# Optimization experiments

Measured on AMD Instinct MI355X. Metric: run time of the kernel, lower is better.

The kernel has to match this reference:

```python
import jax, jax.numpy as jnp
import numpy as np

N_NODES = 50000
N_EDGES = 800000
D_IN = 64
D_OUT = 64


def setup_inputs() -> dict:
    key = jax.random.key(0)
    k1, k2, k3, k4, k5 = jax.random.split(key, 5)
    features = jax.random.normal(k1, (N_NODES, D_IN), dtype=jnp.float32)
    edge_src = jax.random.randint(k2, (N_EDGES,), 0, N_NODES, dtype=jnp.int32)
    edge_dst = jax.random.randint(k3, (N_EDGES,), 0, N_NODES, dtype=jnp.int32)
    edge_weight = jax.random.uniform(k4, (N_EDGES,), dtype=jnp.float32)
    # Linear(2*D_IN, D_OUT): weight [D_OUT, 2*D_IN], bias [D_OUT]
    W = jax.random.normal(k5, (D_OUT, 2 * D_IN), dtype=jnp.float32) * (1.0 / np.sqrt(2 * D_IN))
    b = jnp.zeros((D_OUT,), dtype=jnp.float32)
    return {"features": features, "edge_src": edge_src, "edge_dst": edge_dst,
            "edge_weight": edge_weight, "W": W, "b": b}


def reference(features, edge_src, edge_dst, edge_weight, W, b):
    n = features.shape[0]
    # spmm(adj, features): out[i] = sum_j adj[i,j] * features[j]
    gathered = features[edge_src] * edge_weight[:, None]          # [E, D_IN]
    neighbor = jax.ops.segment_sum(gathered, edge_dst, num_segments=n)  # [N, D_IN]
    combined = jnp.concatenate([features, neighbor], axis=1)     # [N, 2*D_IN]
    out = combined @ W.T + b                                      # [N, D_OUT]
    # F.normalize(p=2, dim=1): x / max(||x||, 1e-12)
    norm = jnp.maximum(jnp.linalg.norm(out, axis=1, keepdims=True), 1e-12)
    return out / norm
```

## Files before the change

### kernel.cpp

```cpp
#include <hip/hip_runtime.h>

#define D 64
#define TILE 1024
#define RB 8
#define EPB 2048
#define EPT 8

__global__ __launch_bounds__(256) void hist_kernel(
    const int* __restrict__ edge_dst, int* __restrict__ deg,
    int n_edges, int n_nodes)
{
    __shared__ int s_cnt;
    __shared__ int s_d[EPB];
    int r = blockIdx.x & (RB - 1);
    int chunk = blockIdx.x >> 3;
    int lo = (int)((long long)r * n_nodes / RB);
    int hi = (int)((long long)(r + 1) * n_nodes / RB);
    if (threadIdx.x == 0) s_cnt = 0;
    __syncthreads();

    int base = chunk * EPB + threadIdx.x * EPT;
    int d[EPT];
    if (base + EPT - 1 < n_edges) {
        int4 v0 = *(const int4*)(edge_dst + base);
        int4 v1 = *(const int4*)(edge_dst + base + 4);
        d[0]=v0.x; d[1]=v0.y; d[2]=v0.z; d[3]=v0.w;
        d[4]=v1.x; d[5]=v1.y; d[6]=v1.z; d[7]=v1.w;
    } else {
        #pragma unroll
        for (int k = 0; k < EPT; ++k)
            d[k] = (base + k < n_edges) ? edge_dst[base + k] : -1;
    }

    int lane = threadIdx.x & 63;
    unsigned long long lt = (lane == 63) ? ~0ull >> 1
                                         : ((1ull << (lane + 1)) - 1) >> 1;
    #pragma unroll
    for (int k = 0; k < EPT; ++k) {
        bool m = (d[k] >= lo && d[k] < hi);
        unsigned long long bal = __ballot(m);
        int cw = __popcll(bal);
        if (cw) {
            int bs = 0;
            if (lane == 0) bs = atomicAdd(&s_cnt, cw);
            bs = __builtin_amdgcn_readfirstlane(bs);
            if (m) s_d[bs + __popcll(bal & lt)] = d[k];
        }
    }
    __syncthreads();
    int c = s_cnt;
    for (int i = threadIdx.x; i < c; i += 256) atomicAdd(&deg[s_d[i]], 1);
}

__global__ __launch_bounds__(256) void tile_sum_kernel(
    const int* __restrict__ deg, int* __restrict__ partial, int n)
{
    int t = threadIdx.x;
    int base = blockIdx.x * TILE + t * 4;
    int s = 0;
    if (base + 3 < n) {
        int4 v = *(const int4*)(deg + base);
        s = v.x + v.y + v.z + v.w;
    } else {
        for (int k = 0; k < 4; ++k) if (base + k < n) s += deg[base + k];
    }
    #pragma unroll
    for (int off = 1; off < 64; off <<= 1) s += __shfl_xor(s, off, 64);
    __shared__ int wsum[4];
    int lane = t & 63, wv = t >> 6;
    if (lane == 0) wsum[wv] = s;
    __syncthreads();
    if (t == 0) partial[blockIdx.x] = wsum[0] + wsum[1] + wsum[2] + wsum[3];
}

__global__ __launch_bounds__(64) void scan_partial_kernel(
    const int* __restrict__ partial, int* __restrict__ ppref, int nb,
    int* __restrict__ offsets, int n, int n_edges)
{
    int lane = threadIdx.x;
    int carry = 0;
    for (int base = 0; base < nb; base += 64) {
        int idx = base + lane;
        int v = (idx < nb) ? partial[idx] : 0;
        int inc = v;
        #pragma unroll
        for (int off = 1; off < 64; off <<= 1) {
            int u = __shfl_up(inc, off, 64);
            if (lane >= off) inc += u;
        }
        if (idx < nb) ppref[idx] = carry + inc - v;
        carry += __shfl(inc, 63, 64);
    }
    if (lane == 0) offsets[n] = n_edges;
}

__global__ __launch_bounds__(256) void scan_tile_kernel(
    const int* __restrict__ deg, const int* __restrict__ ppref,
    int* __restrict__ offsets, int* __restrict__ cursor, int n)
{
    int t = threadIdx.x;
    int base = blockIdx.x * TILE + t * 4;
    int e0 = 0, e1 = 0, e2 = 0, e3 = 0;
    if (base + 3 < n) {
        int4 v = *(const int4*)(deg + base);
        e0 = v.x; e1 = v.y; e2 = v.z; e3 = v.w;
    } else {
        if (base + 0 < n) e0 = deg[base + 0];
        if (base + 1 < n) e1 = deg[base + 1];
        if (base + 2 < n) e2 = deg[base + 2];
        if (base + 3 < n) e3 = deg[base + 3];
    }
    int s = e0 + e1 + e2 + e3;
    int inc = s;
    int lane = t & 63, wv = t >> 6;
    #pragma unroll
    for (int off = 1; off < 64; off <<= 1) {
        int u = __shfl_up(inc, off, 64);
        if (lane >= off) inc += u;
    }
    __shared__ int wsum[4];
    if (lane == 63) wsum[wv] = inc;
    __syncthreads();
    int wpre = 0;
    for (int wq = 0; wq < wv; ++wq) wpre += wsum[wq];
    int excl = ppref[blockIdx.x] + wpre + inc - s;
    int o0 = excl, o1 = o0 + e0, o2 = o1 + e1, o3 = o2 + e2;
    if (base + 0 < n) { offsets[base + 0] = o0; cursor[base + 0] = o0; }
    if (base + 1 < n) { offsets[base + 1] = o1; cursor[base + 1] = o1; }
    if (base + 2 < n) { offsets[base + 2] = o2; cursor[base + 2] = o2; }
    if (base + 3 < n) { offsets[base + 3] = o3; cursor[base + 3] = o3; }
}

__global__ __launch_bounds__(256) void fill_kernel(
    const int* __restrict__ edge_src, const int* __restrict__ edge_dst,
    const float* __restrict__ edge_weight,
    int* __restrict__ cursor, int2* __restrict__ csr_sw,
    int n_edges, int n_nodes)
{
    __shared__ int s_cnt;
    __shared__ int s_d[EPB];
    __shared__ int s_e[EPB];
    int r = blockIdx.x & (RB - 1);
    int chunk = blockIdx.x >> 3;
    int lo = (int)((long long)r * n_nodes / RB);
    int hi = (int)((long long)(r + 1) * n_nodes / RB);
    if (threadIdx.x == 0) s_cnt = 0;
    __syncthreads();

    int base = chunk * EPB + threadIdx.x * EPT;
    int d[EPT];
    if (base + EPT - 1 < n_edges) {
        int4 v0 = *(const int4*)(edge_dst + base);
        int4 v1 = *(const int4*)(edge_dst + base + 4);
        d[0]=v0.x; d[1]=v0.y; d[2]=v0.z; d[3]=v0.w;
        d[4]=v1.x; d[5]=v1.y; d[6]=v1.z; d[7]=v1.w;
    } else {
        #pragma unroll
        for (int k = 0; k < EPT; ++k)
            d[k] = (base + k < n_edges) ? edge_dst[base + k] : -1;
    }

    int lane = threadIdx.x & 63;
    unsigned long long lt = (lane == 63) ? ~0ull >> 1
                                         : ((1ull << (lane + 1)) - 1) >> 1;
    #pragma unroll
    for (int k = 0; k < EPT; ++k) {
        bool m = (d[k] >= lo && d[k] < hi);
        unsigned long long bal = __ballot(m);
        int cw = __popcll(bal);
        if (cw) {
            int bs = 0;
            if (lane == 0) bs = atomicAdd(&s_cnt, cw);
            bs = __builtin_amdgcn_readfirstlane(bs);
            if (m) {
                int p = bs + __popcll(bal & lt);
                s_d[p] = d[k];
                s_e[p] = base + k;
            }
        }
    }
    __syncthreads();
    int c = s_cnt;
    for (int i = threadIdx.x; i < c; i += 256) {
        int dk = s_d[i];
        int e  = s_e[i];
        int pos = atomicAdd(&cursor[dk], 1);
        csr_sw[pos] = make_int2(edge_src[e], __float_as_int(edge_weight[e]));
    }
}

__global__ __launch_bounds__(256) void gather_kernel(
    const float* __restrict__ features, const int2* __restrict__ csr_sw,
    const int* __restrict__ offsets, float* __restrict__ neighbor, int n_nodes)
{
    int lane = threadIdx.x & 63;
    int gw = (blockIdx.x * 256 + threadIdx.x) >> 6;
    int nw = (gridDim.x * 256) >> 6;
    for (int i = gw; i < n_nodes; i += nw) {
        int beg = __builtin_amdgcn_readfirstlane(offsets[i]);
        int end = __builtin_amdgcn_readfirstlane(offsets[i + 1]);
        float acc = 0.f;
        int j = beg;
        for (; j + 7 < end; j += 8) {
            int2 p[8];
            float a[8];
            #pragma unroll
            for (int q = 0; q < 8; ++q) p[q] = csr_sw[j + q];
            #pragma unroll
            for (int q = 0; q < 8; ++q)
                a[q] = features[(size_t)p[q].x * D + lane];
            #pragma unroll
            for (int q = 0; q < 8; ++q)
                acc = fmaf(__int_as_float(p[q].y), a[q], acc);
        }
        for (; j < end; ++j) {
            int2 p = csr_sw[j];
            acc = fmaf(__int_as_float(p.y), features[(size_t)p.x * D + lane], acc);
        }
        neighbor[(size_t)i * D + lane] = acc;
    }
}

__global__ __launch_bounds__(128) void wtrans_kernel(
    const float* __restrict__ W, float* __restrict__ Wt)
{
    int idx = blockIdx.x * 128 + threadIdx.x;
    if (idx < 64 * 128) {
        int o = idx >> 7, k = idx & 127;
        Wt[k * 64 + o] = W[idx];
    }
}

__global__ __launch_bounds__(64) void gemm_norm_kernel(
    const float* __restrict__ features, const float* __restrict__ neighbor,
    const float* __restrict__ Wt,
    const float* __restrict__ bias,
    float* __restrict__ out, int n_nodes)
{
    __shared__ float Wl[128 * 64];
    int tid = threadIdx.x;
    {
        const float4* src = (const float4*)Wt;
        float4* dst = (float4*)Wl;
        #pragma unroll
        for (int i = 0; i < 32; ++i) dst[tid + i * 64] = src[tid + i * 64];
    }
    __syncthreads();

    int nt = tid & 7;
    int mt = tid >> 3;

    long long i0 = (long long)blockIdx.x * 64;

    int nclamp[8];
    #pragma unroll
    for (int t = 0; t < 8; ++t) {
        long long node = i0 + mt + 8 * t;
        nclamp[t] = (int)((node < n_nodes) ? node : (n_nodes - 1));
    }

    float acc[8][8];
    #pragma unroll
    for (int t = 0; t < 8; ++t)
        #pragma unroll
        for (int j = 0; j < 8; ++j) acc[t][j] = 0.f;

    #pragma unroll
    for (int h = 0; h < 2; ++h) {
        const float* __restrict__ A = (h == 0) ? features : neighbor;
        #pragma unroll 1
        for (int k4 = 0; k4 < 16; ++k4) {
            float4 a4[8];
            #pragma unroll
            for (int t = 0; t < 8; ++t)
                a4[t] = *(const float4*)(A + (size_t)nclamp[t] * D + k4 * 4);
            int kk = h * 64 + k4 * 4;
            float4 b0[4], b1[4];
            #pragma unroll
            for (int i = 0; i < 4; ++i) {
                const float* wrow = Wl + (kk + i) * 64 + nt * 8;
                b0[i] = *(const float4*)(wrow);
                b1[i] = *(const float4*)(wrow + 4);
            }
            #pragma unroll
            for (int t = 0; t < 8; ++t) {
                float av[4] = {a4[t].x, a4[t].y, a4[t].z, a4[t].w};
                #pragma unroll
                for (int i = 0; i < 4; ++i) {
                    acc[t][0] = fmaf(av[i], b0[i].x, acc[t][0]);
                    acc[t][1] = fmaf(av[i], b0[i].y, acc[t][1]);
                    acc[t][2] = fmaf(av[i], b0[i].z, acc[t][2]);
                    acc[t][3] = fmaf(av[i], b0[i].w, acc[t][3]);
                    acc[t][4] = fmaf(av[i], b1[i].x, acc[t][4]);
                    acc[t][5] = fmaf(av[i], b1[i].y, acc[t][5]);
                    acc[t][6] = fmaf(av[i], b1[i].z, acc[t][6]);
                    acc[t][7] = fmaf(av[i], b1[i].w, acc[t][7]);
                }
            }
        }
    }

    float bl[8];
    #pragma unroll
    for (int j = 0; j < 8; ++j) bl[j] = bias[nt * 8 + j];

    #pragma unroll
    for (int t = 0; t < 8; ++t) {
        long long node = i0 + mt + 8 * t;
        float s = 0.f;
        #pragma unroll
        for (int j = 0; j < 8; ++j) {
            acc[t][j] += bl[j];
            s = fmaf(acc[t][j], acc[t][j], s);
        }
        s += __shfl_xor(s, 1, 64);
        s += __shfl_xor(s, 2, 64);
        s += __shfl_xor(s, 4, 64);
        float inv = 1.f / fmaxf(sqrtf(s), 1e-12f);
        if (node < n_nodes) {
            float4 o0 = make_float4(acc[t][0] * inv, acc[t][1] * inv,
                                    acc[t][2] * inv, acc[t][3] * inv);
            float4 o1 = make_float4(acc[t][4] * inv, acc[t][5] * inv,
                                    acc[t][6] * inv, acc[t][7] * inv);
            float* op = out + (size_t)node * D + nt * 8;
            *(float4*)op = o0;
            *(float4*)(op + 4) = o1;
        }
    }
}

extern "C" void kernel_launch(void* const* d_in, const int* in_sizes, int n_in,
                              void* d_out, int out_size, void* d_ws, size_t ws_size,
                              hipStream_t stream) {
    const float* features    = (const float*)d_in[0];
    const int*   edge_src    = (const int*)d_in[1];
    const int*   edge_dst    = (const int*)d_in[2];
    const float* edge_weight = (const float*)d_in[3];
    const float* W           = (const float*)d_in[4];
    const float* b           = (const float*)d_in[5];
    float*       out         = (float*)d_out;

    int n = in_sizes[0] / D;
    int E = in_sizes[1];
    int nb = (n + TILE - 1) / TILE;
    int nchunks = (E + EPB - 1) / EPB;

    char* ws = (char*)d_ws;
    auto al = [](size_t x) { return (x + 255) & ~(size_t)255; };
    size_t o = 0;
    int* deg      = (int*)(ws + o); o += al((size_t)n * 4);
    int* cursor   = (int*)(ws + o); o += al((size_t)n * 4);
    int* offsets  = (int*)(ws + o); o += al((size_t)(n + 1) * 4);
    int* partial  = (int*)(ws + o); o += al((size_t)nb * 4);
    int* ppref    = (int*)(ws + o); o += al((size_t)nb * 4);
    float* Wt     = (float*)(ws + o); o += al((size_t)64 * 128 * 4);
    int2* csr_sw  = (int2*)(ws + o); o += al((size_t)E * 8);
    float* neighbor = (float*)(ws + o);

    hipMemsetAsync(deg, 0, (size_t)n * 4, stream);

    wtrans_kernel<<<64, 128, 0, stream>>>(W, Wt);
    hist_kernel<<<nchunks * RB, 256, 0, stream>>>(edge_dst, deg, E, n);
    tile_sum_kernel<<<nb, 256, 0, stream>>>(deg, partial, n);
    scan_partial_kernel<<<1, 64, 0, stream>>>(partial, ppref, nb, offsets, n, E);
    scan_tile_kernel<<<nb, 256, 0, stream>>>(deg, ppref, offsets, cursor, n);
    fill_kernel<<<nchunks * RB, 256, 0, stream>>>(edge_src, edge_dst, edge_weight,
                                                  cursor, csr_sw, E, n);
    gather_kernel<<<2048, 256, 0, stream>>>(features, csr_sw, offsets,
                                            neighbor, n);
    int gblocks = (n + 63) / 64;
    gemm_norm_kernel<<<gblocks, 64, 0, stream>>>(features, neighbor, Wt, b,
                                                 out, n);
}
```

Baseline: 215.8 us.

## Record per-edge slot in histogram, drop cursor atomics, merge scan, retile GEMM

The histogram pass now keeps the atomicAdd return value as a 16-bit per-edge slot, so the fill pass computes CSR positions as offsets+slot and needs no second round of global atomics on a cursor array. The single-block partial scan kernel is removed, and each scan tile block sums the preceding partials itself. The GEMM+normalize kernel moves from 64-thread blocks with 8 rows per thread to 256-thread blocks with 4 rows per thread, for more parallelism and lower register pressure. The cost is an extra 2-byte-per-edge buffer written and read, and node degree must fit in 16 bits.

```diff
diff --git a/kernel.cpp b/kernel.cpp
--- a/kernel.cpp
+++ b/kernel.cpp
@@ -8,134 +8,7 @@
 
 __global__ __launch_bounds__(256) void hist_kernel(
     const int* __restrict__ edge_dst, int* __restrict__ deg,
-    int n_edges, int n_nodes)
-{
-    __shared__ int s_cnt;
-    __shared__ int s_d[EPB];
-    int r = blockIdx.x & (RB - 1);
-    int chunk = blockIdx.x >> 3;
-    int lo = (int)((long long)r * n_nodes / RB);
-    int hi = (int)((long long)(r + 1) * n_nodes / RB);
-    if (threadIdx.x == 0) s_cnt = 0;
-    __syncthreads();
-
-    int base = chunk * EPB + threadIdx.x * EPT;
-    int d[EPT];
-    if (base + EPT - 1 < n_edges) {
-        int4 v0 = *(const int4*)(edge_dst + base);
-        int4 v1 = *(const int4*)(edge_dst + base + 4);
-        d[0]=v0.x; d[1]=v0.y; d[2]=v0.z; d[3]=v0.w;
-        d[4]=v1.x; d[5]=v1.y; d[6]=v1.z; d[7]=v1.w;
-    } else {
-        #pragma unroll
-        for (int k = 0; k < EPT; ++k)
-            d[k] = (base + k < n_edges) ? edge_dst[base + k] : -1;
-    }
-
-    int lane = threadIdx.x & 63;
-    unsigned long long lt = (lane == 63) ? ~0ull >> 1
-                                         : ((1ull << (lane + 1)) - 1) >> 1;
-    #pragma unroll
-    for (int k = 0; k < EPT; ++k) {
-        bool m = (d[k] >= lo && d[k] < hi);
-        unsigned long long bal = __ballot(m);
-        int cw = __popcll(bal);
-        if (cw) {
-            int bs = 0;
-            if (lane == 0) bs = atomicAdd(&s_cnt, cw);
-            bs = __builtin_amdgcn_readfirstlane(bs);
-            if (m) s_d[bs + __popcll(bal & lt)] = d[k];
-        }
-    }
-    __syncthreads();
-    int c = s_cnt;
-    for (int i = threadIdx.x; i < c; i += 256) atomicAdd(&deg[s_d[i]], 1);
-}
-
-__global__ __launch_bounds__(256) void tile_sum_kernel(
-    const int* __restrict__ deg, int* __restrict__ partial, int n)
-{
-    int t = threadIdx.x;
-    int base = blockIdx.x * TILE + t * 4;
-    int s = 0;
-    if (base + 3 < n) {
-        int4 v = *(const int4*)(deg + base);
-        s = v.x + v.y + v.z + v.w;
-    } else {
-        for (int k = 0; k < 4; ++k) if (base + k < n) s += deg[base + k];
-    }
-    #pragma unroll
-    for (int off = 1; off < 64; off <<= 1) s += __shfl_xor(s, off, 64);
-    __shared__ int wsum[4];
-    int lane = t & 63, wv = t >> 6;
-    if (lane == 0) wsum[wv] = s;
-    __syncthreads();
-    if (t == 0) partial[blockIdx.x] = wsum[0] + wsum[1] + wsum[2] + wsum[3];
-}
-
-__global__ __launch_bounds__(64) void scan_partial_kernel(
-    const int* __restrict__ partial, int* __restrict__ ppref, int nb,
-    int* __restrict__ offsets, int n, int n_edges)
-{
-    int lane = threadIdx.x;
-    int carry = 0;
-    for (int base = 0; base < nb; base += 64) {
-        int idx = base + lane;
-        int v = (idx < nb) ? partial[idx] : 0;
-        int inc = v;
-        #pragma unroll
-        for (int off = 1; off < 64; off <<= 1) {
-            int u = __shfl_up(inc, off, 64);
-            if (lane >= off) inc += u;
-        }
-        if (idx < nb) ppref[idx] = carry + inc - v;
-        carry += __shfl(inc, 63, 64);
-    }
-    if (lane == 0) offsets[n] = n_edges;
-}
-
-__global__ __launch_bounds__(256) void scan_tile_kernel(
-    const int* __restrict__ deg, const int* __restrict__ ppref,
-    int* __restrict__ offsets, int* __restrict__ cursor, int n)
-{
-    int t = threadIdx.x;
-    int base = blockIdx.x * TILE + t * 4;
-    int e0 = 0, e1 = 0, e2 = 0, e3 = 0;
-    if (base + 3 < n) {
-        int4 v = *(const int4*)(deg + base);
-        e0 = v.x; e1 = v.y; e2 = v.z; e3 = v.w;
-    } else {
-        if (base + 0 < n) e0 = deg[base + 0];
-        if (base + 1 < n) e1 = deg[base + 1];
-        if (base + 2 < n) e2 = deg[base + 2];
-        if (base + 3 < n) e3 = deg[base + 3];
-    }
-    int s = e0 + e1 + e2 + e3;
-    int inc = s;
-    int lane = t & 63, wv = t >> 6;
-    #pragma unroll
-    for (int off = 1; off < 64; off <<= 1) {
-        int u = __shfl_up(inc, off, 64);
-        if (lane >= off) inc += u;
-    }
-    __shared__ int wsum[4];
-    if (lane == 63) wsum[wv] = inc;
-    __syncthreads();
-    int wpre = 0;
-    for (int wq = 0; wq < wv; ++wq) wpre += wsum[wq];
-    int excl = ppref[blockIdx.x] + wpre + inc - s;
-    int o0 = excl, o1 = o0 + e0, o2 = o1 + e1, o3 = o2 + e2;
-    if (base + 0 < n) { offsets[base + 0] = o0; cursor[base + 0] = o0; }
-    if (base + 1 < n) { offsets[base + 1] = o1; cursor[base + 1] = o1; }
-    if (base + 2 < n) { offsets[base + 2] = o2; cursor[base + 2] = o2; }
-    if (base + 3 < n) { offsets[base + 3] = o3; cursor[base + 3] = o3; }
-}
-
-__global__ __launch_bounds__(256) void fill_kernel(
-    const int* __restrict__ edge_src, const int* __restrict__ edge_dst,
-    const float* __restrict__ edge_weight,
-    int* __restrict__ cursor, int2* __restrict__ csr_sw,
-    int n_edges, int n_nodes)
+    unsigned short* __restrict__ slot, int n_edges, int n_nodes)
 {
     __shared__ int s_cnt;
     __shared__ int s_d[EPB];
@@ -182,9 +55,131 @@
     __syncthreads();
     int c = s_cnt;
     for (int i = threadIdx.x; i < c; i += 256) {
+        int old = atomicAdd(&deg[s_d[i]], 1);
+        slot[s_e[i]] = (unsigned short)old;
+    }
+}
+
+__global__ __launch_bounds__(256) void tile_sum_kernel(
+    const int* __restrict__ deg, int* __restrict__ partial, int n)
+{
+    int t = threadIdx.x;
+    int base = blockIdx.x * TILE + t * 4;
+    int s = 0;
+    if (base + 3 < n) {
+        int4 v = *(const int4*)(deg + base);
+        s = v.x + v.y + v.z + v.w;
+    } else {
+        for (int k = 0; k < 4; ++k) if (base + k < n) s += deg[base + k];
+    }
+    #pragma unroll
+    for (int off = 1; off < 64; off <<= 1) s += __shfl_xor(s, off, 64);
+    __shared__ int wsum[4];
+    int lane = t & 63, wv = t >> 6;
+    if (lane == 0) wsum[wv] = s;
+    __syncthreads();
+    if (t == 0) partial[blockIdx.x] = wsum[0] + wsum[1] + wsum[2] + wsum[3];
+}
+
+__global__ __launch_bounds__(256) void scan_tile_kernel(
+    const int* __restrict__ deg, const int* __restrict__ partial,
+    int* __restrict__ offsets, int n, int n_edges)
+{
+    int t = threadIdx.x;
+    int lane = t & 63, wv = t >> 6;
+
+    int bp = 0;
+    for (int j = lane; j < blockIdx.x; j += 64) bp += partial[j];
+    #pragma unroll
+    for (int off = 1; off < 64; off <<= 1) bp += __shfl_xor(bp, off, 64);
+
+    int base = blockIdx.x * TILE + t * 4;
+    int e0 = 0, e1 = 0, e2 = 0, e3 = 0;
+    if (base + 3 < n) {
+        int4 v = *(const int4*)(deg + base);
+        e0 = v.x; e1 = v.y; e2 = v.z; e3 = v.w;
+    } else {
+        if (base + 0 < n) e0 = deg[base + 0];
+        if (base + 1 < n) e1 = deg[base + 1];
+        if (base + 2 < n) e2 = deg[base + 2];
+        if (base + 3 < n) e3 = deg[base + 3];
+    }
+    int s = e0 + e1 + e2 + e3;
+    int inc = s;
+    #pragma unroll
+    for (int off = 1; off < 64; off <<= 1) {
+        int u = __shfl_up(inc, off, 64);
+        if (lane >= off) inc += u;
+    }
+    __shared__ int wsum[4];
+    if (lane == 63) wsum[wv] = inc;
+    __syncthreads();
+    int wpre = 0;
+    for (int wq = 0; wq < wv; ++wq) wpre += wsum[wq];
+    int excl = bp + wpre + inc - s;
+    int o0 = excl, o1 = o0 + e0, o2 = o1 + e1, o3 = o2 + e2;
+    if (base + 0 < n) offsets[base + 0] = o0;
+    if (base + 1 < n) offsets[base + 1] = o1;
+    if (base + 2 < n) offsets[base + 2] = o2;
+    if (base + 3 < n) offsets[base + 3] = o3;
+    if (blockIdx.x == 0 && t == 0) offsets[n] = n_edges;
+}
+
+__global__ __launch_bounds__(256) void fill_kernel(
+    const int* __restrict__ edge_src, const int* __restrict__ edge_dst,
+    const float* __restrict__ edge_weight,
+    const unsigned short* __restrict__ slot,
+    const int* __restrict__ offsets, int2* __restrict__ csr_sw,
+    int n_edges, int n_nodes)
+{
+    __shared__ int s_cnt;
+    __shared__ int s_d[EPB];
+    __shared__ int s_e[EPB];
+    int r = blockIdx.x & (RB - 1);
+    int chunk = blockIdx.x >> 3;
+    int lo = (int)((long long)r * n_nodes / RB);
+    int hi = (int)((long long)(r + 1) * n_nodes / RB);
+    if (threadIdx.x == 0) s_cnt = 0;
+    __syncthreads();
+
+    int base = chunk * EPB + threadIdx.x * EPT;
+    int d[EPT];
+    if (base + EPT - 1 < n_edges) {
+        int4 v0 = *(const int4*)(edge_dst + base);
+        int4 v1 = *(const int4*)(edge_dst + base + 4);
+        d[0]=v0.x; d[1]=v0.y; d[2]=v0.z; d[3]=v0.w;
+        d[4]=v1.x; d[5]=v1.y; d[6]=v1.z; d[7]=v1.w;
+    } else {
+        #pragma unroll
+        for (int k = 0; k < EPT; ++k)
+            d[k] = (base + k < n_edges) ? edge_dst[base + k] : -1;
+    }
+
+    int lane = threadIdx.x & 63;
+    unsigned long long lt = (lane == 63) ? ~0ull >> 1
+                                         : ((1ull << (lane + 1)) - 1) >> 1;
+    #pragma unroll
+    for (int k = 0; k < EPT; ++k) {
+        bool m = (d[k] >= lo && d[k] < hi);
+        unsigned long long bal = __ballot(m);
+        int cw = __popcll(bal);
+        if (cw) {
+            int bs = 0;
+            if (lane == 0) bs = atomicAdd(&s_cnt, cw);
+            bs = __builtin_amdgcn_readfirstlane(bs);
+            if (m) {
+                int p = bs + __popcll(bal & lt);
+                s_d[p] = d[k];
+                s_e[p] = base + k;
+            }
+        }
+    }
+    __syncthreads();
+    int c = s_cnt;
+    for (int i = threadIdx.x; i < c; i += 256) {
         int dk = s_d[i];
         int e  = s_e[i];
-        int pos = atomicAdd(&cursor[dk], 1);
+        int pos = offsets[dk] + (int)slot[e];
         csr_sw[pos] = make_int2(edge_src[e], __float_as_int(edge_weight[e]));
     }
 }
@@ -231,7 +226,8 @@
     }
 }
 
-__global__ __launch_bounds__(64) void gemm_norm_kernel(
+#define MT 4
+__global__ __launch_bounds__(256) void gemm_norm_kernel(
     const float* __restrict__ features, const float* __restrict__ neighbor,
     const float* __restrict__ Wt,
     const float* __restrict__ bias,
@@ -243,25 +239,27 @@
         const float4* src = (const float4*)Wt;
         float4* dst = (float4*)Wl;
         #pragma unroll
-        for (int i = 0; i < 32; ++i) dst[tid + i * 64] = src[tid + i * 64];
-    }
-    __syncthreads();
-
-    int nt = tid & 7;
-    int mt = tid >> 3;
-
-    long long i0 = (long long)blockIdx.x * 64;
-
-    int nclamp[8];
-    #pragma unroll
-    for (int t = 0; t < 8; ++t) {
+        for (int i = 0; i < 8; ++i) dst[tid + i * 256] = src[tid + i * 256];
+    }
+    __syncthreads();
+
+    int lane = tid & 63;
+    int wv = tid >> 6;
+    int nt = lane & 7;
+    int mt = lane >> 3;
+
+    long long i0 = (long long)blockIdx.x * (4 * 8 * MT) + wv * (8 * MT);
+
+    int nclamp[MT];
+    #pragma unroll
+    for (int t = 0; t < MT; ++t) {
         long long node = i0 + mt + 8 * t;
         nclamp[t] = (int)((node < n_nodes) ? node : (n_nodes - 1));
     }
 
-    float acc[8][8];
-    #pragma unroll
-    for (int t = 0; t < 8; ++t)
+    float acc[MT][8];
+    #pragma unroll
+    for (int t = 0; t < MT; ++t)
         #pragma unroll
         for (int j = 0; j < 8; ++j) acc[t][j] = 0.f;
 
@@ -270,9 +268,9 @@
         const float* __restrict__ A = (h == 0) ? features : neighbor;
         #pragma unroll 1
         for (int k4 = 0; k4 < 16; ++k4) {
-            float4 a4[8];
-            #pragma unroll
-            for (int t = 0; t < 8; ++t)
+            float4 a4[MT];
+            #pragma unroll
+            for (int t = 0; t < MT; ++t)
                 a4[t] = *(const float4*)(A + (size_t)nclamp[t] * D + k4 * 4);
             int kk = h * 64 + k4 * 4;
             float4 b0[4], b1[4];
@@ -283,7 +281,7 @@
                 b1[i] = *(const float4*)(wrow + 4);
             }
             #pragma unroll
-            for (int t = 0; t < 8; ++t) {
+            for (int t = 0; t < MT; ++t) {
                 float av[4] = {a4[t].x, a4[t].y, a4[t].z, a4[t].w};
                 #pragma unroll
                 for (int i = 0; i < 4; ++i) {
@@ -305,7 +303,7 @@
     for (int j = 0; j < 8; ++j) bl[j] = bias[nt * 8 + j];
 
     #pragma unroll
-    for (int t = 0; t < 8; ++t) {
+    for (int t = 0; t < MT; ++t) {
         long long node = i0 + mt + 8 * t;
         float s = 0.f;
         #pragma unroll
@@ -349,10 +347,9 @@
     auto al = [](size_t x) { return (x + 255) & ~(size_t)255; };
     size_t o = 0;
     int* deg      = (int*)(ws + o); o += al((size_t)n * 4);
-    int* cursor   = (int*)(ws + o); o += al((size_t)n * 4);
     int* offsets  = (int*)(ws + o); o += al((size_t)(n + 1) * 4);
     int* partial  = (int*)(ws + o); o += al((size_t)nb * 4);
-    int* ppref    = (int*)(ws + o); o += al((size_t)nb * 4);
+    unsigned short* slot = (unsigned short*)(ws + o); o += al((size_t)E * 2);
     float* Wt     = (float*)(ws + o); o += al((size_t)64 * 128 * 4);
     int2* csr_sw  = (int2*)(ws + o); o += al((size_t)E * 8);
     float* neighbor = (float*)(ws + o);
@@ -360,15 +357,14 @@
     hipMemsetAsync(deg, 0, (size_t)n * 4, stream);
 
     wtrans_kernel<<<64, 128, 0, stream>>>(W, Wt);
-    hist_kernel<<<nchunks * RB, 256, 0, stream>>>(edge_dst, deg, E, n);
+    hist_kernel<<<nchunks * RB, 256, 0, stream>>>(edge_dst, deg, slot, E, n);
     tile_sum_kernel<<<nb, 256, 0, stream>>>(deg, partial, n);
-    scan_partial_kernel<<<1, 64, 0, stream>>>(partial, ppref, nb, offsets, n, E);
-    scan_tile_kernel<<<nb, 256, 0, stream>>>(deg, ppref, offsets, cursor, n);
+    scan_tile_kernel<<<nb, 256, 0, stream>>>(deg, partial, offsets, n, E);
     fill_kernel<<<nchunks * RB, 256, 0, stream>>>(edge_src, edge_dst, edge_weight,
-                                                  cursor, csr_sw, E, n);
+                                                  slot, offsets, csr_sw, E, n);
     gather_kernel<<<2048, 256, 0, stream>>>(features, csr_sw, offsets,
                                             neighbor, n);
-    int gblocks = (n + 63) / 64;
-    gemm_norm_kernel<<<gblocks, 64, 0, stream>>>(features, neighbor, Wt, b,
-                                                 out, n);
-}
+    int gblocks = (n + 4 * 8 * MT - 1) / (4 * 8 * MT);
+    gemm_norm_kernel<<<gblocks, 256, 0, stream>>>(features, neighbor, Wt, b,
+                                                  out, n);
+}
```

After: 186.1 us. 13.8% less time.
